# Kernel optimization log

Hardware: AMD Instinct MI355X
Metric: run time of the kernel (lower is better)

Reference implementation:

```python
import jax, jax.numpy as jnp
import numpy as np

D_MODEL = 1024
N_HEADS = 16
D_K = D_MODEL // N_HEADS


def _xavier(key, shape):
    fan_in, fan_out = shape[1], shape[0]
    a = np.sqrt(6.0 / (fan_in + fan_out))
    return jax.random.uniform(key, shape, jnp.float32, -a, a)


def setup_inputs() -> dict:
    key = jax.random.key(0)
    kx, kq, kk, kv, ko = jax.random.split(key, 5)
    x = jax.random.normal(kx, (2, 2048, D_MODEL), jnp.float32)
    # nn.Linear weights are [out, in]; y = x @ W.T
    Wq = _xavier(kq, (D_MODEL, D_MODEL))
    Wk = _xavier(kk, (D_MODEL, D_MODEL))
    Wv = _xavier(kv, (D_MODEL, D_MODEL))
    Wo = _xavier(ko, (D_MODEL, D_MODEL))
    bo = jnp.zeros((D_MODEL,), jnp.float32)
    return {"x": x, "Wq": Wq, "Wk": Wk, "Wv": Wv, "Wo": Wo, "bo": bo}


def reference(x, Wq, Wk, Wv, Wo, bo):
    B, S, D = x.shape
    def split_heads(t):
        # [B,S,D] -> [B,H,S,d_k]
        return t.reshape(B, S, N_HEADS, D_K).transpose(0, 2, 1, 3)
    Q = split_heads(x @ Wq.T)
    K = split_heads(x @ Wk.T)
    V = split_heads(x @ Wv.T)
    scale = 1.0 / jnp.sqrt(jnp.asarray(D_K, x.dtype))
    scores = jnp.einsum('bhqd,bhkd->bhqk', Q, K) * scale  # [B,H,S,S]
    attn = jax.nn.softmax(scores, axis=-1)
    out = jnp.einsum('bhqk,bhkd->bhqd', attn, V)  # [B,H,S,d_k]
    out = out.transpose(0, 2, 1, 3).reshape(B, S, D)  # merge heads
    return out @ Wo.T + bo
```

## Files before the change

kernel.cpp:

```cpp
#include <hip/hip_runtime.h>


typedef __attribute__((ext_vector_type(8))) short bf16x8;
typedef __attribute__((ext_vector_type(4))) short bf16x4;
typedef __attribute__((ext_vector_type(4))) float f32x4;
typedef __attribute__((ext_vector_type(2))) unsigned int u32x2;
typedef __attribute__((ext_vector_type(4))) unsigned int u32x4;

#define GK 1024
#define SEQ 2048
#define NHEAD 16
#define DKD 64
#define PADW 72

#define MFMA32(a, b, c) __builtin_amdgcn_mfma_f32_16x16x32_bf16((a), (b), (c), 0, 0, 0)

#if __has_builtin(__builtin_amdgcn_exp2f)
#define EXP2(x) __builtin_amdgcn_exp2f(x)
#else
#define EXP2(x) exp2f(x)
#endif

#define QSCALE 0.18033688011f

static __device__ __forceinline__ unsigned short f2bf(float f) {
    unsigned int u = __float_as_uint(f);
    u += 0x7fffu + ((u >> 16) & 1u);
    return (unsigned short)(u >> 16);
}

static __device__ __forceinline__ unsigned int pack_bf2(float a, float b) {
    unsigned int ua = __float_as_uint(a) + 0x8000u;
    unsigned int ub = __float_as_uint(b) + 0x8000u;
    return __builtin_amdgcn_perm(ub, ua, 0x07060302u);
}

__global__ __launch_bounds__(256) void cast_all(const float* __restrict__ x,
                                                const float* __restrict__ wq,
                                                const float* __restrict__ wk,
                                                const float* __restrict__ wv,
                                                const float* __restrict__ wo,
                                                unsigned short* __restrict__ Xb,
                                                unsigned short* __restrict__ Wqkv,
                                                unsigned short* __restrict__ Wob) {
    const int bid = blockIdx.x;
    const float* src; unsigned short* dst; int off;
    if (bid < 4096)      { src = x;  dst = Xb;             off = bid; }
    else if (bid < 5120) { src = wq; dst = Wqkv;           off = bid - 4096; }
    else if (bid < 6144) { src = wk; dst = Wqkv + 1048576; off = bid - 5120; }
    else if (bid < 7168) { src = wv; dst = Wqkv + 2097152; off = bid - 6144; }
    else                 { src = wo; dst = Wob;            off = bid - 7168; }
    const int i = off * 1024 + threadIdx.x * 4;
    float4 v = *(const float4*)(src + i);
    u32x2 p; p.x = pack_bf2(v.x, v.y); p.y = pack_bf2(v.z, v.w);
    *(u32x2*)(dst + i) = p;
}

template <int MODE, int BN>
__global__ __launch_bounds__(256) void gemm_bt(const unsigned short* __restrict__ A,
                                               const unsigned short* __restrict__ Bw,
                                               unsigned short* __restrict__ outb,
                                               float* __restrict__ outf,
                                               const float* __restrict__ bias) {
    constexpr int NJ = BN / 32;
    constexpr int LOOP_BYTES = 128 * 64 * 2 + BN * 64 * 2;
    constexpr int EPI_BYTES  = 4 * 64 * PADW * 2;
    constexpr int SMEM_BYTES = (MODE == 0)
        ? (LOOP_BYTES > EPI_BYTES ? LOOP_BYTES : EPI_BYTES)
        : LOOP_BYTES;
    __shared__ __align__(16) unsigned char SMEM[SMEM_BYTES];
    unsigned short* As = (unsigned short*)SMEM;
    unsigned short* Bs = As + 128 * 64;

    const int t    = threadIdx.x;
    const int lane = t & 63;
    const int w    = t >> 6;
    const int wm   = (w >> 1) * 64;
    const int wn   = (w & 1) * (BN / 2);
    const int bm0  = blockIdx.x * 128;
    const int bn0  = blockIdx.y * BN;
    const int lm   = lane & 15;
    const int lq   = lane >> 4;
    const int swzb = lm & 7;

    const unsigned short* Ab = A + (size_t)bm0 * GK;
    const unsigned short* Bb = Bw + (size_t)bn0 * GK;

    f32x4 acc[4][NJ];
    const f32x4 Z4 = {0.f, 0.f, 0.f, 0.f};
#pragma unroll
    for (int i = 0; i < 4; i++)
#pragma unroll
        for (int j = 0; j < NJ; j++) acc[i][j] = Z4;

    const int q_uni = (t & ~63);

    for (int k0 = 0; k0 < GK; k0 += 64) {
        __syncthreads();
#pragma unroll
        for (int i = 0; i < 4; ++i) {
            int q  = i * 256 + t;
            int r  = q >> 3;
            int gc = (q & 7) ^ (r & 7);
            int q0 = i * 256 + q_uni;
            __builtin_amdgcn_global_load_lds(
                (const __attribute__((address_space(1))) void*)(Ab + (size_t)r * GK + k0 + gc * 8),
                (__attribute__((address_space(3))) void*)(As + (size_t)q0 * 8),
                16, 0, 0);
        }
#pragma unroll
        for (int i = 0; i < BN / 32; ++i) {
            int q  = i * 256 + t;
            int r  = q >> 3;
            int gc = (q & 7) ^ (r & 7);
            int q0 = i * 256 + q_uni;
            __builtin_amdgcn_global_load_lds(
                (const __attribute__((address_space(1))) void*)(Bb + (size_t)r * GK + k0 + gc * 8),
                (__attribute__((address_space(3))) void*)(Bs + (size_t)q0 * 8),
                16, 0, 0);
        }
        __syncthreads();

#pragma unroll
        for (int kk = 0; kk < 2; ++kk) {
            const int swz = ((kk * 4 + lq) ^ swzb) * 8;
            bf16x8 af[4], bf[NJ];
#pragma unroll
            for (int i = 0; i < 4; i++)
                af[i] = *(const bf16x8*)(As + (wm + i * 16 + lm) * 64 + swz);
#pragma unroll
            for (int j = 0; j < NJ; j++)
                bf[j] = *(const bf16x8*)(Bs + (wn + j * 16 + lm) * 64 + swz);
#pragma unroll
            for (int i = 0; i < 4; i++)
#pragma unroll
                for (int j = 0; j < NJ; j++)
                    acc[i][j] = MFMA32(af[i], bf[j], acc[i][j]);
        }
    }

    if (MODE == 0) {
        __syncthreads();
        unsigned short* E  = (unsigned short*)SMEM;
        unsigned short* Ew = E + w * (64 * PADW);
        const int nbase = bn0 + wn;
        const int which = nbase >> 10;
        const int hh    = (nbase & 1023) >> 6;
        if (which != 2) {
            const float sc = (which == 0) ? QSCALE : 1.0f;
#pragma unroll
            for (int i = 0; i < 4; i++)
#pragma unroll
                for (int j = 0; j < 4; j++)
#pragma unroll
                    for (int r = 0; r < 4; r++)
                        Ew[(i * 16 + lq * 4 + r) * PADW + j * 16 + lm] =
                            f2bf(acc[i][j][r] * sc);
            unsigned short* dst = outb + (size_t)which * 4194304;
#pragma unroll
            for (int rep = 0; rep < 8; ++rep) {
                const int mm = rep * 8 + (lane >> 3);
                const int d0 = (lane & 7) * 8;
                uint4 v = *(const uint4*)(Ew + mm * PADW + d0);
                const int m_g = bm0 + wm + mm;
                const int b = m_g >> 11, s = m_g & 2047;
                *(uint4*)(dst + (((size_t)(b * NHEAD + hh)) * SEQ + s) * DKD + d0) = v;
            }
        } else {
#pragma unroll
            for (int i = 0; i < 4; i++)
#pragma unroll
                for (int j = 0; j < 4; j++) {
                    u32x2 pk;
                    pk.x = pack_bf2(acc[i][j][0], acc[i][j][1]);
                    pk.y = pack_bf2(acc[i][j][2], acc[i][j][3]);
                    *(u32x2*)(Ew + (j * 16 + lm) * PADW + i * 16 + lq * 4) = pk;
                }
            unsigned short* dst = outb + (size_t)2 * 4194304;
#pragma unroll
            for (int rep = 0; rep < 8; ++rep) {
                const int nn = rep * 8 + (lane >> 3);
                const int mc = (lane & 7) * 8;
                uint4 v = *(const uint4*)(Ew + nn * PADW + mc);
                const int m_g = bm0 + wm + mc;
                const int b = m_g >> 11, s0 = m_g & 2047;
                *(uint4*)(dst + (((size_t)(b * NHEAD + hh)) * DKD + nn) * SEQ + s0) = v;
            }
        }
    } else {
#pragma unroll
        for (int i = 0; i < 4; i++) {
            const int mbase = bm0 + wm + i * 16 + lq * 4;
#pragma unroll
            for (int j = 0; j < NJ; j++) {
                const int n = bn0 + wn + j * 16 + lm;
#pragma unroll
                for (int r = 0; r < 4; r++)
                    outf[(size_t)(mbase + r) * 1024 + n] = acc[i][j][r] + bias[n];
            }
        }
    }
}

__global__ __launch_bounds__(256, 2) void attn_kernel(const unsigned short* __restrict__ Qg,
                                                      const unsigned short* __restrict__ Kg,
                                                      const unsigned short* __restrict__ Vtg,
                                                      unsigned short* __restrict__ Og) {
    __shared__ __align__(16) unsigned short KV[2][2][64 * PADW];

    const int id  = blockIdx.x;
    const int xcd = id & 7;
    const int j8  = id >> 3;
    const int bh  = xcd * 4 + (j8 & 3);
    const int qb  = j8 >> 2;
    const unsigned short* Qp  = Qg  + ((size_t)bh * SEQ + qb * 128) * DKD;
    const unsigned short* Kp  = Kg  + (size_t)bh * SEQ * DKD;
    const unsigned short* Vtp = Vtg + (size_t)bh * DKD * SEQ;

    const int t    = threadIdx.x;
    const int lane = t & 63;
    const int w    = t >> 6;
    const int qg   = w >> 1;
    const int kg   = w & 1;
    const int lm   = lane & 15;
    const int kq   = lane >> 4;

    const f32x4 Z4 = {0.f, 0.f, 0.f, 0.f};

    bf16x8 aq[2][2][2];
#pragma unroll
    for (int h2 = 0; h2 < 2; ++h2)
#pragma unroll
        for (int c = 0; c < 2; ++c)
#pragma unroll
            for (int kk = 0; kk < 2; ++kk)
                aq[h2][c][kk] = *(const bf16x8*)(Qp + (size_t)(h2 * 64 + qg * 32 + c * 16 + lm) * DKD + kk * 32 + kq * 8);

    f32x4 o[2][2][4];
    float ls[2][2];
#pragma unroll
    for (int h2 = 0; h2 < 2; ++h2)
#pragma unroll
        for (int c = 0; c < 2; ++c) {
            ls[h2][c] = 0.f;
#pragma unroll
            for (int dj = 0; dj < 4; ++dj) o[h2][c][dj] = Z4;
        }

    const int sr = t >> 2, sc = (t & 3) * 16;
    uint4 kreg0, kreg1, vreg0, vreg1;
    {
        const unsigned short* kp = Kp + (size_t)sr * DKD + sc;
        const unsigned short* vp = Vtp + (size_t)sr * SEQ + sc;
        uint4 a0 = *(const uint4*)(kp), a1 = *(const uint4*)(kp + 8);
        uint4 b0 = *(const uint4*)(vp), b1 = *(const uint4*)(vp + 8);
        uint4* dk = (uint4*)(&KV[0][0][sr * PADW + sc]); dk[0] = a0; dk[1] = a1;
        uint4* dv = (uint4*)(&KV[0][1][sr * PADW + sc]); dv[0] = b0; dv[1] = b1;
    }
    {
        const unsigned short* kp = Kp + (size_t)(64 + sr) * DKD + sc;
        kreg0 = *(const uint4*)(kp); kreg1 = *(const uint4*)(kp + 8);
        const unsigned short* vp = Vtp + (size_t)sr * SEQ + 64 + sc;
        vreg0 = *(const uint4*)(vp); vreg1 = *(const uint4*)(vp + 8);
    }

    for (int kt = 0; kt < 32; ++kt) {
        asm volatile("s_waitcnt lgkmcnt(0)\n\ts_barrier" ::: "memory");
        const unsigned short* Kc = &KV[kt & 1][0][0];
        const unsigned short* Vc = &KV[kt & 1][1][0];

        bf16x8 ak[2][2];
#pragma unroll
        for (int kc = 0; kc < 2; ++kc)
#pragma unroll
            for (int kk = 0; kk < 2; ++kk)
                ak[kc][kk] = *(const bf16x8*)(Kc + (kg * 32 + kc * 16 + lm) * PADW + kk * 32 + kq * 8);

        if (kt + 1 < 32) {
            uint4* dk = (uint4*)(&KV[(kt + 1) & 1][0][sr * PADW + sc]);
            dk[0] = kreg0; dk[1] = kreg1;
            uint4* dv = (uint4*)(&KV[(kt + 1) & 1][1][sr * PADW + sc]);
            dv[0] = vreg0; dv[1] = vreg1;
        }
        if (kt + 2 < 32) {
            const unsigned short* kp = Kp + (size_t)((kt + 2) * 64 + sr) * DKD + sc;
            kreg0 = *(const uint4*)(kp); kreg1 = *(const uint4*)(kp + 8);
            const unsigned short* vp = Vtp + (size_t)sr * SEQ + (kt + 2) * 64 + sc;
            vreg0 = *(const uint4*)(vp); vreg1 = *(const uint4*)(vp + 8);
        }

        bf16x8 bv[4];
#pragma unroll
        for (int dj = 0; dj < 4; ++dj) {
            const unsigned short* vr = Vc + (dj * 16 + lm) * PADW + kg * 32;
            u32x2 lo = __builtin_bit_cast(u32x2, *(const bf16x4*)(vr + kq * 4));
            u32x2 hi = __builtin_bit_cast(u32x2, *(const bf16x4*)(vr + 16 + kq * 4));
            u32x4 uu; uu.x = lo.x; uu.y = lo.y; uu.z = hi.x; uu.w = hi.y;
            bv[dj] = __builtin_bit_cast(bf16x8, uu);
        }

#pragma unroll
        for (int h2 = 0; h2 < 2; ++h2) {
            f32x4 s[2][2];
            __builtin_amdgcn_s_setprio(1);
#pragma unroll
            for (int kc = 0; kc < 2; ++kc)
#pragma unroll
                for (int c = 0; c < 2; ++c) {
                    s[kc][c] = MFMA32(ak[kc][0], aq[h2][c][0], Z4);
                    s[kc][c] = MFMA32(ak[kc][1], aq[h2][c][1], s[kc][c]);
                }
            __builtin_amdgcn_s_setprio(0);

#pragma unroll
            for (int c = 0; c < 2; ++c) {
#pragma unroll
                for (int kc = 0; kc < 2; ++kc)
#pragma unroll
                    for (int r = 0; r < 4; ++r) s[kc][c][r] = EXP2(s[kc][c][r]);
                ls[h2][c] += ((s[0][c][0] + s[0][c][1]) + (s[0][c][2] + s[0][c][3]))
                           + ((s[1][c][0] + s[1][c][1]) + (s[1][c][2] + s[1][c][3]));
            }

            bf16x8 pa[2];
#pragma unroll
            for (int c = 0; c < 2; ++c) {
                u32x4 uu;
                uu.x = pack_bf2(s[0][c][0], s[0][c][1]);
                uu.y = pack_bf2(s[0][c][2], s[0][c][3]);
                uu.z = pack_bf2(s[1][c][0], s[1][c][1]);
                uu.w = pack_bf2(s[1][c][2], s[1][c][3]);
                pa[c] = __builtin_bit_cast(bf16x8, uu);
            }

            __builtin_amdgcn_s_setprio(1);
#pragma unroll
            for (int dj = 0; dj < 4; ++dj)
#pragma unroll
                for (int c = 0; c < 2; ++c)
                    o[h2][c][dj] = MFMA32(pa[c], bv[dj], o[h2][c][dj]);
            __builtin_amdgcn_s_setprio(0);
        }
    }

    __syncthreads();
    float* Lf = (float*)(&KV[0][0][0]);

#pragma unroll
    for (int h2 = 0; h2 < 2; ++h2)
#pragma unroll
        for (int c = 0; c < 2; ++c) {
            float v = ls[h2][c];
            v += __shfl_xor(v, 16);
            v += __shfl_xor(v, 32);
            if (kq == 0) Lf[(h2 * 4 + w) * 32 + c * 16 + lm] = v;
        }
    __syncthreads();

    const int rq = t >> 2;
    const int dq = (t & 3) * 8;
    const int qgr = rq >> 5, qlr = rq & 31;
    float li[2];
#pragma unroll
    for (int h2 = 0; h2 < 2; ++h2) {
        float l = Lf[(h2 * 4 + qgr * 2) * 32 + qlr] + Lf[(h2 * 4 + qgr * 2 + 1) * 32 + qlr];
#if __has_builtin(__builtin_amdgcn_rcpf)
        li[h2] = __builtin_amdgcn_rcpf(l);
#else
        li[h2] = 1.0f / l;
#endif
    }
    __syncthreads();

    const int b = bh >> 4, h = bh & 15;
#pragma unroll
    for (int p = 0; p < 2; ++p) {
#pragma unroll
        for (int h2 = 0; h2 < 2; ++h2)
#pragma unroll
            for (int c = 0; c < 2; ++c)
#pragma unroll
                for (int djh = 0; djh < 2; ++djh) {
                    const int dj = 2 * p + djh;
#pragma unroll
                    for (int r = 0; r < 4; ++r)
                        Lf[((h2 * 4 + w) * 32 + c * 16 + kq * 4 + r) * 36 + djh * 16 + lm] = o[h2][c][dj][r];
                }
        __syncthreads();
#pragma unroll
        for (int h2 = 0; h2 < 2; ++h2) {
            const int rowA = ((h2 * 4 + qgr * 2) * 32 + qlr) * 36;
            const int rowB = ((h2 * 4 + qgr * 2 + 1) * 32 + qlr) * 36;
            f32x4 a0 = *(const f32x4*)(Lf + rowA + dq) + *(const f32x4*)(Lf + rowB + dq);
            f32x4 a1 = *(const f32x4*)(Lf + rowA + dq + 4) + *(const f32x4*)(Lf + rowB + dq + 4);
            uint4 outv;
            outv.x = pack_bf2(a0[0] * li[h2], a0[1] * li[h2]);
            outv.y = pack_bf2(a0[2] * li[h2], a0[3] * li[h2]);
            outv.z = pack_bf2(a1[0] * li[h2], a1[1] * li[h2]);
            outv.w = pack_bf2(a1[2] * li[h2], a1[3] * li[h2]);
            *(uint4*)(Og + (((size_t)(b * SEQ + qb * 128 + h2 * 64 + rq)) * NHEAD + h) * DKD + p * 32 + dq) = outv;
        }
        __syncthreads();
    }
}

extern "C" void kernel_launch(void* const* d_in, const int* in_sizes, int n_in,
                              void* d_out, int out_size, void* d_ws, size_t ws_size,
                              hipStream_t stream) {
    const float* x  = (const float*)d_in[0];
    const float* Wq = (const float*)d_in[1];
    const float* Wk = (const float*)d_in[2];
    const float* Wv = (const float*)d_in[3];
    const float* Wo = (const float*)d_in[4];
    const float* bo = (const float*)d_in[5];
    float* out = (float*)d_out;

    unsigned short* ws = (unsigned short*)d_ws;
    unsigned short* Xb   = ws;
    unsigned short* Wqkv = ws + 4194304;
    unsigned short* Wob  = ws + 7340032;
    unsigned short* QKV  = ws + 8388608;
    unsigned short* Ob   = ws + 20971520;

    cast_all<<<8192, 256, 0, stream>>>(x, Wq, Wk, Wv, Wo, Xb, Wqkv, Wob);
    gemm_bt<0, 128><<<dim3(32, 24), 256, 0, stream>>>(Xb, Wqkv, QKV, nullptr, nullptr);
    attn_kernel<<<512, 256, 0, stream>>>(QKV, QKV + 4194304, QKV + 8388608, Ob);
    gemm_bt<1, 64><<<dim3(32, 16), 256, 0, stream>>>(Ob, Wob, nullptr, out, bo);
}
```

Baseline: 181.5 us.

## Double-buffer GEMM LDS tiles with K-step 32 and prefetch

Replaces the single-buffered 64-wide K tile loop with two 32-wide LDS buffers. The next tile is issued via global_load_lds while MFMAs run on the current one, and the swizzle is changed to match the 4-chunk rows. This aims to hide global-to-LDS latency behind compute and drops one of the two barriers per iteration. In exchange it doubles the iteration count, halving MFMA work per barrier. Buffer reuse correctness also now relies on the single barrier at loop top, since the load into Nxt is issued right after it.

```diff
diff --git a/kernel.cpp b/kernel.cpp
--- a/kernel.cpp
+++ b/kernel.cpp
@@ -63,14 +63,15 @@
                                                float* __restrict__ outf,
                                                const float* __restrict__ bias) {
     constexpr int NJ = BN / 32;
-    constexpr int LOOP_BYTES = 128 * 64 * 2 + BN * 64 * 2;
+    constexpr int TILE = (128 + BN) * 32;
+    constexpr int LOOP_BYTES = 2 * TILE * 2;
     constexpr int EPI_BYTES  = 4 * 64 * PADW * 2;
     constexpr int SMEM_BYTES = (MODE == 0)
         ? (LOOP_BYTES > EPI_BYTES ? LOOP_BYTES : EPI_BYTES)
         : LOOP_BYTES;
     __shared__ __align__(16) unsigned char SMEM[SMEM_BYTES];
-    unsigned short* As = (unsigned short*)SMEM;
-    unsigned short* Bs = As + 128 * 64;
+    unsigned short* Buf0 = (unsigned short*)SMEM;
+    unsigned short* Buf1 = Buf0 + TILE;
 
     const int t    = threadIdx.x;
     const int lane = t & 63;
@@ -81,7 +82,7 @@
     const int bn0  = blockIdx.y * BN;
     const int lm   = lane & 15;
     const int lq   = lane >> 4;
-    const int swzb = lm & 7;
+    const int swz  = (lq ^ (lm & 3)) * 8;
 
     const unsigned short* Ab = A + (size_t)bm0 * GK;
     const unsigned short* Bb = Bw + (size_t)bn0 * GK;
@@ -95,48 +96,50 @@
 
     const int q_uni = (t & ~63);
 
-    for (int k0 = 0; k0 < GK; k0 += 64) {
-        __syncthreads();
-#pragma unroll
-        for (int i = 0; i < 4; ++i) {
+    auto STAGE = [&](unsigned short* Bp, int k0) {
+#pragma unroll
+        for (int i = 0; i < 2; ++i) {
             int q  = i * 256 + t;
-            int r  = q >> 3;
-            int gc = (q & 7) ^ (r & 7);
+            int r  = q >> 2;
+            int gc = (q & 3) ^ (r & 3);
             int q0 = i * 256 + q_uni;
             __builtin_amdgcn_global_load_lds(
                 (const __attribute__((address_space(1))) void*)(Ab + (size_t)r * GK + k0 + gc * 8),
-                (__attribute__((address_space(3))) void*)(As + (size_t)q0 * 8),
+                (__attribute__((address_space(3))) void*)(Bp + (size_t)q0 * 8),
                 16, 0, 0);
         }
 #pragma unroll
-        for (int i = 0; i < BN / 32; ++i) {
+        for (int i = 0; i < BN / 64; ++i) {
             int q  = i * 256 + t;
-            int r  = q >> 3;
-            int gc = (q & 7) ^ (r & 7);
+            int r  = q >> 2;
+            int gc = (q & 3) ^ (r & 3);
             int q0 = i * 256 + q_uni;
             __builtin_amdgcn_global_load_lds(
                 (const __attribute__((address_space(1))) void*)(Bb + (size_t)r * GK + k0 + gc * 8),
-                (__attribute__((address_space(3))) void*)(Bs + (size_t)q0 * 8),
+                (__attribute__((address_space(3))) void*)(Bp + 128 * 32 + (size_t)q0 * 8),
                 16, 0, 0);
         }
+    };
+
+    STAGE(Buf0, 0);
+    for (int ks = 0; ks < GK / 32; ++ks) {
         __syncthreads();
-
-#pragma unroll
-        for (int kk = 0; kk < 2; ++kk) {
-            const int swz = ((kk * 4 + lq) ^ swzb) * 8;
-            bf16x8 af[4], bf[NJ];
-#pragma unroll
-            for (int i = 0; i < 4; i++)
-                af[i] = *(const bf16x8*)(As + (wm + i * 16 + lm) * 64 + swz);
+        unsigned short* Cur = (ks & 1) ? Buf1 : Buf0;
+        unsigned short* Nxt = (ks & 1) ? Buf0 : Buf1;
+        if (ks + 1 < GK / 32) STAGE(Nxt, (ks + 1) * 32);
+
+        bf16x8 af[4], bf[NJ];
+#pragma unroll
+        for (int i = 0; i < 4; i++)
+            af[i] = *(const bf16x8*)(Cur + (wm + i * 16 + lm) * 32 + swz);
+#pragma unroll
+        for (int j = 0; j < NJ; j++)
+            bf[j] = *(const bf16x8*)(Cur + 128 * 32 + (wn + j * 16 + lm) * 32 + swz);
+#pragma unroll
+        for (int i = 0; i < 4; i++)
 #pragma unroll
             for (int j = 0; j < NJ; j++)
-                bf[j] = *(const bf16x8*)(Bs + (wn + j * 16 + lm) * 64 + swz);
-#pragma unroll
-            for (int i = 0; i < 4; i++)
-#pragma unroll
-                for (int j = 0; j < NJ; j++)
-                    acc[i][j] = MFMA32(af[i], bf[j], acc[i][j]);
-        }
+                acc[i][j] = MFMA32(af[i], bf[j], acc[i][j]);
     }
 
     if (MODE == 0) {
@@ -146,6 +149,7 @@
         const int nbase = bn0 + wn;
         const int which = nbase >> 10;
         const int hh    = (nbase & 1023) >> 6;
+        const int lq4   = lq * 4;
         if (which != 2) {
             const float sc = (which == 0) ? QSCALE : 1.0f;
 #pragma unroll
@@ -154,7 +158,7 @@
                 for (int j = 0; j < 4; j++)
 #pragma unroll
                     for (int r = 0; r < 4; r++)
-                        Ew[(i * 16 + lq * 4 + r) * PADW + j * 16 + lm] =
+                        Ew[(i * 16 + lq4 + r) * PADW + j * 16 + lm] =
                             f2bf(acc[i][j][r] * sc);
             unsigned short* dst = outb + (size_t)which * 4194304;
 #pragma unroll
@@ -174,7 +178,7 @@
                     u32x2 pk;
                     pk.x = pack_bf2(acc[i][j][0], acc[i][j][1]);
                     pk.y = pack_bf2(acc[i][j][2], acc[i][j][3]);
-                    *(u32x2*)(Ew + (j * 16 + lm) * PADW + i * 16 + lq * 4) = pk;
+                    *(u32x2*)(Ew + (j * 16 + lm) * PADW + i * 16 + lq4) = pk;
                 }
             unsigned short* dst = outb + (size_t)2 * 4194304;
 #pragma unroll
```

Result: faster. 176.9 us (median of 2 runs) (-2.6%).
